# Kernel optimization log

Hardware: AMD Instinct MI355X
Metric: run time of the kernel (lower is better)

## Reference

```python
import jax, jax.numpy as jnp
import numpy as np

N_NODES = 100000
N_EDGES = 1600000
IN_F, HID_F, OUT_F = 64, 64, 16


def setup_inputs() -> dict:
    key = jax.random.key(0)
    k_x, k_e, k_w1, k_w2 = jax.random.split(key, 4)
    x = jax.random.normal(k_x, (N_NODES, IN_F), dtype=jnp.float32)
    edge_index = jax.random.randint(k_e, (2, N_EDGES), 0, N_NODES, dtype=jnp.int64)
    # Glorot-ish init for the GCNConv linear weights; bias zeros (PyG default)
    W1 = jax.random.normal(k_w1, (IN_F, HID_F), dtype=jnp.float32) / np.sqrt(IN_F)
    b1 = jnp.zeros((HID_F,), dtype=jnp.float32)
    W2 = jax.random.normal(k_w2, (HID_F, OUT_F), dtype=jnp.float32) / np.sqrt(HID_F)
    b2 = jnp.zeros((OUT_F,), dtype=jnp.float32)
    return {"x": x, "edge_index": edge_index, "W1": W1, "b1": b1, "W2": W2, "b2": b2}


def reference(x, edge_index, W1, b1, W2, b2):
    N = x.shape[0]
    # GCNConv: add self-loops, symmetric normalization D^-1/2 A D^-1/2
    loop = jnp.arange(N, dtype=edge_index.dtype)
    src = jnp.concatenate([edge_index[0], loop])  # [E+N]
    dst = jnp.concatenate([edge_index[1], loop])  # [E+N]
    deg = jax.ops.segment_sum(jnp.ones_like(dst, dtype=x.dtype), dst, num_segments=N)
    dis = jax.lax.rsqrt(deg)  # deg >= 1 due to self-loops
    norm = dis[src] * dis[dst]  # [E+N]

    def gcn_conv(h, W, b):
        h = h @ W                                   # [N, d_out]
        msg = h[src] * norm[:, None]                # gather + scale  [E+N, d_out]
        agg = jax.ops.segment_sum(msg, dst, num_segments=N)  # scatter-add
        return agg + b

    h = jax.nn.relu(gcn_conv(x, W1, b1))
    h = gcn_conv(h, W2, b2)
    return jax.nn.log_softmax(h, axis=1)
```

## Files before the change

kernel.cpp:

```cpp
#include <hip/hip_runtime.h>
#include <hip/hip_bf16.h>
#include <hip/hip_fp16.h>


#define F1 64
#define F2 16
#define NBKT 256
#define BSH 512
#define NPB 256
#define SBD 1024
#define STG 9216

typedef _Float16 f16x8 __attribute__((ext_vector_type(8)));
typedef _Float16 f16x4 __attribute__((ext_vector_type(4)));
typedef float f32x2 __attribute__((ext_vector_type(2)));
typedef float f32x4 __attribute__((ext_vector_type(4)));
typedef float f32x8 __attribute__((ext_vector_type(8)));

__device__ inline f32x8 shfl_xor_f32x8(f32x8 v, int off) {
  f32x8 r;
#pragma unroll
  for (int k = 0; k < 8; ++k) r[k] = __shfl_xor(v[k], off);
  return r;
}
__device__ inline f32x4 shfl_xor_f32x4(f32x4 v, int off) {
  f32x4 r;
#pragma unroll
  for (int k = 0; k < 4; ++k) r[k] = __shfl_xor(v[k], off);
  return r;
}

__device__ inline void acc_fp8x8(f32x2* a, uint2 v) {
  a[0] += __builtin_amdgcn_cvt_pk_f32_fp8((int)v.x, false);
  a[1] += __builtin_amdgcn_cvt_pk_f32_fp8((int)v.x, true);
  a[2] += __builtin_amdgcn_cvt_pk_f32_fp8((int)v.y, false);
  a[3] += __builtin_amdgcn_cvt_pk_f32_fp8((int)v.y, true);
}

__global__ void k_w(const float* __restrict__ W1, const float* __restrict__ W2,
                    const float* __restrict__ b1,
                    __half* __restrict__ W1T, __half* __restrict__ W2Tp,
                    float* __restrict__ b1p, int* __restrict__ bcur, int nb) {
  int t = threadIdx.x;
  for (int i = t; i < 64 * 64; i += 256) {
    int n = i >> 6, k = i & 63;
    W1T[i] = __float2half(W1[k * 64 + n]);
  }
  for (int i = t; i < 16 * 64; i += 256) {
    int j = i >> 6, p = i & 63;
    int fp = 16 * (p & 3) + (p >> 2);
    W2Tp[i] = __float2half(W2[fp * 16 + j]);
  }
  if (t < 64) b1p[t] = b1[16 * (t & 3) + (t >> 2)];
  if (t < nb) bcur[t] = t * STG;
}

__global__ void k_bscatter(const int* __restrict__ src, const int* __restrict__ dst,
                           int* __restrict__ bcur, int* __restrict__ tmp,
                           int E, int nb, int chunk) {
  __shared__ int h[NBKT];
  __shared__ int cur[NBKT];
  int t = threadIdx.x, sb = blockIdx.x;
  int beg = sb * chunk, end = min(beg + chunk, E);
  if (t < NBKT) h[t] = 0;
  __syncthreads();
  int e;
  for (e = beg + t * 4; e + 4 <= end; e += 4 * SBD) {
    int4 d4 = *(const int4*)(dst + e);
    atomicAdd(&h[d4.x >> 9], 1);
    atomicAdd(&h[d4.y >> 9], 1);
    atomicAdd(&h[d4.z >> 9], 1);
    atomicAdd(&h[d4.w >> 9], 1);
  }
  for (; e < end; ++e) atomicAdd(&h[dst[e] >> 9], 1);
  __syncthreads();
  if (t < nb) cur[t] = atomicAdd(&bcur[t], h[t]);
  __syncthreads();
  for (e = beg + t * 4; e + 4 <= end; e += 4 * SBD) {
    int4 d4 = *(const int4*)(dst + e);
    int4 s4 = *(const int4*)(src + e);
    int b, off;
    b = d4.x >> 9; off = atomicAdd(&cur[b], 1); tmp[off] = (s4.x << 9) | (d4.x & 511);
    b = d4.y >> 9; off = atomicAdd(&cur[b], 1); tmp[off] = (s4.y << 9) | (d4.y & 511);
    b = d4.z >> 9; off = atomicAdd(&cur[b], 1); tmp[off] = (s4.z << 9) | (d4.z & 511);
    b = d4.w >> 9; off = atomicAdd(&cur[b], 1); tmp[off] = (s4.w << 9) | (d4.w & 511);
  }
  for (; e < end; ++e) {
    int d = dst[e];
    int b = d >> 9;
    int off = atomicAdd(&cur[b], 1);
    tmp[off] = (src[e] << 9) | (d & 511);
  }
}

__global__ void k_cg2(const int* __restrict__ tmp, const int* __restrict__ bcur,
                      int* __restrict__ csr, int* __restrict__ rowptr,
                      float* __restrict__ dis,
                      const float* __restrict__ x, const __half* __restrict__ W1T,
                      unsigned char* __restrict__ h1, int N, int nb) {
  __shared__ int stage[STG];
  __shared__ int sc[BSH];
  __shared__ int cnt[BSH];
  __shared__ int lofs[BSH];
  __shared__ float dnode[BSH];
  int b = blockIdx.x, t = threadIdx.x;
  int lenb = bcur[b] - b * STG;
  if (t < NBKT) sc[t] = (t < nb) ? (bcur[t] - t * STG) : 0;
  __syncthreads();
  for (int off = 1; off < NBKT; off <<= 1) {
    int a = (t < NBKT && t >= off) ? sc[t - off] : 0;
    __syncthreads();
    if (t < NBKT) sc[t] += a;
    __syncthreads();
  }
  int beg = (b == 0) ? 0 : sc[b - 1];
  __syncthreads();
  int s0 = b * STG;
  int lim = lenb & ~3;
  for (int i = t * 4; i < lim; i += 4 * BSH)
    *(int4*)(stage + i) = *(const int4*)(tmp + s0 + i);
  {
    int r = lim + t;
    if (r < lenb) stage[r] = tmp[s0 + r];
  }
  cnt[t] = 0;
  __syncthreads();
  for (int i = t; i < lenb; i += BSH) atomicAdd(&cnt[stage[i] & (BSH - 1)], 1);
  __syncthreads();
  sc[t] = cnt[t];
  __syncthreads();
  for (int off = 1; off < BSH; off <<= 1) {
    int a = (t >= off) ? sc[t - off] : 0;
    __syncthreads();
    sc[t] += a;
    __syncthreads();
  }
  int excl = (t == 0) ? 0 : sc[t - 1];
  lofs[t] = excl;
  int n = b * BSH + t;
  float dn_t = rsqrtf((float)(cnt[t] + 1));
  dnode[t] = dn_t;
  if (n <= N) rowptr[n] = beg + excl;
  if (n < N) dis[n] = dn_t;
  cnt[t] = 0;
  __syncthreads();
  for (int i = t; i < lenb; i += BSH) {
    int p = stage[i];
    int l = p & (BSH - 1);
    int off = atomicAdd(&cnt[l], 1);
    csr[beg + lofs[l] + off] = p >> 9;
  }
  int wv = t >> 6, lane = t & 63;
  int m = lane & 15, q = lane >> 4;
  const _Float16* wt = (const _Float16*)W1T;
  f16x8 bf[4][2];
#pragma unroll
  for (int c = 0; c < 4; ++c)
#pragma unroll
    for (int kt = 0; kt < 2; ++kt)
      bf[c][kt] = *(const f16x8*)&wt[(c * 16 + m) * 64 + kt * 32 + q * 8];
#pragma unroll
  for (int it = 0; it < 4; ++it) {
    int lrow0 = wv * 64 + it * 16;
    int row0 = b * BSH + lrow0;
    int arow = min(row0 + m, N - 1);
    f16x8 a[2];
#pragma unroll
    for (int kt = 0; kt < 2; ++kt) {
      const float4* xp = (const float4*)(x + (size_t)arow * 64 + kt * 32 + q * 8);
      float4 u = xp[0], v = xp[1];
      a[kt][0] = (_Float16)u.x; a[kt][1] = (_Float16)u.y;
      a[kt][2] = (_Float16)u.z; a[kt][3] = (_Float16)u.w;
      a[kt][4] = (_Float16)v.x; a[kt][5] = (_Float16)v.y;
      a[kt][6] = (_Float16)v.z; a[kt][7] = (_Float16)v.w;
    }
    f32x4 acc[4] = {};
#pragma unroll
    for (int kt = 0; kt < 2; ++kt)
#pragma unroll
      for (int c = 0; c < 4; ++c)
        acc[c] = __builtin_amdgcn_mfma_f32_16x16x32_f16(a[kt], bf[c][kt], acc[c], 0, 0, 0);
#pragma unroll
    for (int r = 0; r < 4; ++r) {
      int lr = lrow0 + q * 4 + r;
      int nn = b * BSH + lr;
      if (nn < N) {
        float dn = dnode[lr];
        int d = __builtin_amdgcn_cvt_pk_fp8_f32(acc[0][r] * dn, acc[1][r] * dn, 0, false);
        d = __builtin_amdgcn_cvt_pk_fp8_f32(acc[2][r] * dn, acc[3][r] * dn, d, true);
        *(unsigned int*)(h1 + (size_t)nn * 64 + m * 4) = (unsigned)d;
      }
    }
  }
}

__global__ void k_agg1f(const unsigned char* __restrict__ h, const float* __restrict__ dis,
                        const int* __restrict__ rowptr, const int* __restrict__ csr,
                        const float* __restrict__ b1p, const __half* __restrict__ W2Tp,
                        __half* __restrict__ h2, int N) {
  int gt = blockIdx.x * blockDim.x + threadIdx.x;
  int w = gt >> 6;
  int lane = gt & 63;
  int half = lane >> 5;
  int sub = (lane >> 3) & 3;
  int fl = lane & 7;
  int n = w * 2 + half;
  if (n >= N) return;
  float dn = dis[n];
  float4 bu = *(const float4*)(b1p + fl * 8);
  float4 bv = *(const float4*)(b1p + fl * 8 + 4);
  const _Float16* wt = (const _Float16*)W2Tp;
  f16x8 wj[4];
#pragma unroll
  for (int i = 0; i < 4; ++i)
    wj[i] = *(const f16x8*)&wt[(sub * 4 + i) * 64 + fl * 8];
  f32x2 a0[4] = {}, a1[4] = {};
  if (sub == 0)
    acc_fp8x8(a0, *(const uint2*)&h[(size_t)n * 64 + fl * 8]);
  int beg = rowptr[n], end = rowptr[n + 1];
  int e = beg + sub;
  int sA = (e < end) ? csr[e] : -1;
  int sB = (e + 4 < end) ? csr[e + 4] : -1;
  while (sB >= 0) {
    int e2 = e + 8;
    int sC = (e2 < end) ? csr[e2] : -1;
    int sD = (e2 + 4 < end) ? csr[e2 + 4] : -1;
    uint2 v0 = *(const uint2*)&h[(size_t)sA * 64 + fl * 8];
    uint2 v1 = *(const uint2*)&h[(size_t)sB * 64 + fl * 8];
    acc_fp8x8(a0, v0);
    acc_fp8x8(a1, v1);
    sA = sC; sB = sD; e = e2;
  }
  if (sA >= 0)
    acc_fp8x8(a0, *(const uint2*)&h[(size_t)sA * 64 + fl * 8]);
  f32x8 acc;
#pragma unroll
  for (int k = 0; k < 4; ++k) {
    f32x2 s = a0[k] + a1[k];
    acc[2 * k] = s[0];
    acc[2 * k + 1] = s[1];
  }
  acc += shfl_xor_f32x8(acc, 8);
  acc += shfl_xor_f32x8(acc, 16);
  float bb[8] = {bu.x, bu.y, bu.z, bu.w, bv.x, bv.y, bv.z, bv.w};
  float hr[8];
#pragma unroll
  for (int k = 0; k < 8; ++k)
    hr[k] = fmaxf(fmaf(dn, acc[k], bb[k]), 0.f);
  float p[4];
#pragma unroll
  for (int i = 0; i < 4; ++i) {
    float s = 0.f;
#pragma unroll
    for (int k = 0; k < 8; ++k) s = fmaf(hr[k], (float)wj[i][k], s);
    s += __shfl_xor(s, 1);
    s += __shfl_xor(s, 2);
    s += __shfl_xor(s, 4);
    p[i] = s;
  }
  if (fl == 0) {
    f16x4 o;
#pragma unroll
    for (int i = 0; i < 4; ++i) o[i] = (_Float16)(p[i] * dn);
    *(f16x4*)((_Float16*)h2 + (size_t)n * 16 + sub * 4) = o;
  }
}

__global__ void k_agg2(const __half* __restrict__ h2, const float* __restrict__ dis,
                       const int* __restrict__ rowptr, const int* __restrict__ csr,
                       const float* __restrict__ b2, float* __restrict__ out, int N) {
  int gt = blockIdx.x * blockDim.x + threadIdx.x;
  int w = gt >> 6;
  int lane = gt & 63;
  int half = lane >> 5;
  int sub = (lane >> 2) & 7;
  int fl = lane & 3;
  int n = w * 2 + half;
  if (n >= N) return;
  const _Float16* hp = (const _Float16*)h2;
  f32x4 acc0 = {}, acc1 = {};
  if (sub == 0)
    acc0 = __builtin_convertvector(*(const f16x4*)&hp[(size_t)n * 16 + fl * 4], f32x4);
  int beg = rowptr[n], end = rowptr[n + 1];
  int e = beg + sub;
  int sA = (e < end) ? csr[e] : -1;
  int sB = (e + 8 < end) ? csr[e + 8] : -1;
  while (sB >= 0) {
    int e2 = e + 16;
    int sC = (e2 < end) ? csr[e2] : -1;
    int sD = (e2 + 8 < end) ? csr[e2 + 8] : -1;
    f16x4 v0 = *(const f16x4*)&hp[(size_t)sA * 16 + fl * 4];
    f16x4 v1 = *(const f16x4*)&hp[(size_t)sB * 16 + fl * 4];
    acc0 += __builtin_convertvector(v0, f32x4);
    acc1 += __builtin_convertvector(v1, f32x4);
    sA = sC; sB = sD; e = e2;
  }
  if (sA >= 0)
    acc0 += __builtin_convertvector(*(const f16x4*)&hp[(size_t)sA * 16 + fl * 4], f32x4);
  f32x4 acc = acc0 + acc1;
  acc += shfl_xor_f32x4(acc, 4);
  acc += shfl_xor_f32x4(acc, 8);
  acc += shfl_xor_f32x4(acc, 16);
  if (sub == 0) {
    float dn = dis[n];
    float4 bb = *(const float4*)(b2 + fl * 4);
    float v0 = fmaf(dn, acc[0], bb.x);
    float v1 = fmaf(dn, acc[1], bb.y);
    float v2 = fmaf(dn, acc[2], bb.z);
    float v3 = fmaf(dn, acc[3], bb.w);
    float m = fmaxf(fmaxf(v0, v1), fmaxf(v2, v3));
    m = fmaxf(m, __shfl_xor(m, 1));
    m = fmaxf(m, __shfl_xor(m, 2));
    float s2 = __expf(v0 - m) + __expf(v1 - m) + __expf(v2 - m) + __expf(v3 - m);
    s2 += __shfl_xor(s2, 1);
    s2 += __shfl_xor(s2, 2);
    float ls = m + __logf(s2);
    float4 o = {v0 - ls, v1 - ls, v2 - ls, v3 - ls};
    *(float4*)(out + (size_t)n * 16 + fl * 4) = o;
  }
}

extern "C" void kernel_launch(void* const* d_in, const int* in_sizes, int n_in,
                              void* d_out, int out_size, void* d_ws, size_t ws_size,
                              hipStream_t stream) {
  const float* x = (const float*)d_in[0];
  const int* ei = (const int*)d_in[1];
  const float* W1 = (const float*)d_in[2];
  const float* b1 = (const float*)d_in[3];
  const float* W2 = (const float*)d_in[4];
  const float* b2 = (const float*)d_in[5];
  float* out = (float*)d_out;

  int N = in_sizes[0] / F1;
  int E = in_sizes[1] / 2;
  const int* src = ei;
  const int* dst = ei + E;
  int nb = (N + BSH - 1) >> 9;
  int chunk = ((E + NPB - 1) / NPB + 3) & ~3;

  char* ws = (char*)d_ws;
  size_t o_w1t = 0;
  size_t o_w2t = o_w1t + 64 * 64 * 2;
  size_t o_b1p = (o_w2t + 16 * 64 * 2 + 255) & ~(size_t)255;
  size_t o_bcur = (o_b1p + 64 * 4 + 255) & ~(size_t)255;
  size_t o_dis = (o_bcur + NBKT * 4 + 255) & ~(size_t)255;
  size_t o_rowp = (o_dis + (size_t)N * 4 + 255) & ~(size_t)255;
  size_t o_tmp = (o_rowp + (size_t)(N + 1) * 4 + 255) & ~(size_t)255;
  size_t o_csr = (o_tmp + (size_t)nb * STG * 4 + 255) & ~(size_t)255;
  size_t o_h1 = (o_csr + (size_t)E * 4 + 255) & ~(size_t)255;
  size_t o_h2 = (o_h1 + (size_t)N * 64 + 255) & ~(size_t)255;

  __half* W1T = (__half*)(ws + o_w1t);
  __half* W2Tp = (__half*)(ws + o_w2t);
  float* b1p = (float*)(ws + o_b1p);
  int* bcur = (int*)(ws + o_bcur);
  float* dis = (float*)(ws + o_dis);
  int* rowptr = (int*)(ws + o_rowp);
  int* tmp = (int*)(ws + o_tmp);
  int* csr = (int*)(ws + o_csr);
  unsigned char* h1 = (unsigned char*)(ws + o_h1);
  __half* h2 = (__half*)(ws + o_h2);

  k_w<<<1, 256, 0, stream>>>(W1, W2, b1, W1T, W2Tp, b1p, bcur, nb);
  k_bscatter<<<NPB, SBD, 0, stream>>>(src, dst, bcur, tmp, E, nb, chunk);
  k_cg2<<<nb, BSH, 0, stream>>>(tmp, bcur, csr, rowptr, dis, x, W1T, h1, N, nb);
  int aw = (N + 1) / 2;
  k_agg1f<<<((size_t)aw * 64 + 255) / 256, 256, 0, stream>>>(h1, dis, rowptr, csr, b1p, W2Tp, h2, N);
  k_agg2<<<((size_t)aw * 64 + 255) / 256, 256, 0, stream>>>(h2, dis, rowptr, csr, b2, out, N);
}
```

Before: 182.9 us.

## Run X·W1 GEMM as extra blocks of the bucket-scatter kernel, rescale later

The layer-1 feature transform (x @ W1 via MFMA, stored as fp8) moves out of the CSR-build kernel. It now runs in extra blocks appended to the edge bucket-scatter launch, so the x reads overlap with the atomic-heavy scatter. Because degrees are not known yet, h1 is stored unscaled, and the CSR kernel later reads h1 back, multiplies each row by its dis value and re-quantizes to fp8 in place. This adds an extra read and write pass over h1 and a second fp8 rounding.

```diff
diff --git a/kernel.cpp b/kernel.cpp
--- a/kernel.cpp
+++ b/kernel.cpp
@@ -55,115 +55,26 @@
   if (t < nb) bcur[t] = t * STG;
 }
 
-__global__ void k_bscatter(const int* __restrict__ src, const int* __restrict__ dst,
-                           int* __restrict__ bcur, int* __restrict__ tmp,
-                           int E, int nb, int chunk) {
-  __shared__ int h[NBKT];
-  __shared__ int cur[NBKT];
+__global__ void k_sg(const int* __restrict__ src, const int* __restrict__ dst,
+                     int* __restrict__ bcur, int* __restrict__ tmp,
+                     int E, int nb, int chunk,
+                     const float* __restrict__ x, const __half* __restrict__ W1T,
+                     unsigned char* __restrict__ h1, int N) {
   int t = threadIdx.x, sb = blockIdx.x;
-  int beg = sb * chunk, end = min(beg + chunk, E);
-  if (t < NBKT) h[t] = 0;
-  __syncthreads();
-  int e;
-  for (e = beg + t * 4; e + 4 <= end; e += 4 * SBD) {
-    int4 d4 = *(const int4*)(dst + e);
-    atomicAdd(&h[d4.x >> 9], 1);
-    atomicAdd(&h[d4.y >> 9], 1);
-    atomicAdd(&h[d4.z >> 9], 1);
-    atomicAdd(&h[d4.w >> 9], 1);
-  }
-  for (; e < end; ++e) atomicAdd(&h[dst[e] >> 9], 1);
-  __syncthreads();
-  if (t < nb) cur[t] = atomicAdd(&bcur[t], h[t]);
-  __syncthreads();
-  for (e = beg + t * 4; e + 4 <= end; e += 4 * SBD) {
-    int4 d4 = *(const int4*)(dst + e);
-    int4 s4 = *(const int4*)(src + e);
-    int b, off;
-    b = d4.x >> 9; off = atomicAdd(&cur[b], 1); tmp[off] = (s4.x << 9) | (d4.x & 511);
-    b = d4.y >> 9; off = atomicAdd(&cur[b], 1); tmp[off] = (s4.y << 9) | (d4.y & 511);
-    b = d4.z >> 9; off = atomicAdd(&cur[b], 1); tmp[off] = (s4.z << 9) | (d4.z & 511);
-    b = d4.w >> 9; off = atomicAdd(&cur[b], 1); tmp[off] = (s4.w << 9) | (d4.w & 511);
-  }
-  for (; e < end; ++e) {
-    int d = dst[e];
-    int b = d >> 9;
-    int off = atomicAdd(&cur[b], 1);
-    tmp[off] = (src[e] << 9) | (d & 511);
-  }
-}
-
-__global__ void k_cg2(const int* __restrict__ tmp, const int* __restrict__ bcur,
-                      int* __restrict__ csr, int* __restrict__ rowptr,
-                      float* __restrict__ dis,
-                      const float* __restrict__ x, const __half* __restrict__ W1T,
-                      unsigned char* __restrict__ h1, int N, int nb) {
-  __shared__ int stage[STG];
-  __shared__ int sc[BSH];
-  __shared__ int cnt[BSH];
-  __shared__ int lofs[BSH];
-  __shared__ float dnode[BSH];
-  int b = blockIdx.x, t = threadIdx.x;
-  int lenb = bcur[b] - b * STG;
-  if (t < NBKT) sc[t] = (t < nb) ? (bcur[t] - t * STG) : 0;
-  __syncthreads();
-  for (int off = 1; off < NBKT; off <<= 1) {
-    int a = (t < NBKT && t >= off) ? sc[t - off] : 0;
-    __syncthreads();
-    if (t < NBKT) sc[t] += a;
-    __syncthreads();
-  }
-  int beg = (b == 0) ? 0 : sc[b - 1];
-  __syncthreads();
-  int s0 = b * STG;
-  int lim = lenb & ~3;
-  for (int i = t * 4; i < lim; i += 4 * BSH)
-    *(int4*)(stage + i) = *(const int4*)(tmp + s0 + i);
-  {
-    int r = lim + t;
-    if (r < lenb) stage[r] = tmp[s0 + r];
-  }
-  cnt[t] = 0;
-  __syncthreads();
-  for (int i = t; i < lenb; i += BSH) atomicAdd(&cnt[stage[i] & (BSH - 1)], 1);
-  __syncthreads();
-  sc[t] = cnt[t];
-  __syncthreads();
-  for (int off = 1; off < BSH; off <<= 1) {
-    int a = (t >= off) ? sc[t - off] : 0;
-    __syncthreads();
-    sc[t] += a;
-    __syncthreads();
-  }
-  int excl = (t == 0) ? 0 : sc[t - 1];
-  lofs[t] = excl;
-  int n = b * BSH + t;
-  float dn_t = rsqrtf((float)(cnt[t] + 1));
-  dnode[t] = dn_t;
-  if (n <= N) rowptr[n] = beg + excl;
-  if (n < N) dis[n] = dn_t;
-  cnt[t] = 0;
-  __syncthreads();
-  for (int i = t; i < lenb; i += BSH) {
-    int p = stage[i];
-    int l = p & (BSH - 1);
-    int off = atomicAdd(&cnt[l], 1);
-    csr[beg + lofs[l] + off] = p >> 9;
-  }
-  int wv = t >> 6, lane = t & 63;
-  int m = lane & 15, q = lane >> 4;
-  const _Float16* wt = (const _Float16*)W1T;
-  f16x8 bf[4][2];
-#pragma unroll
-  for (int c = 0; c < 4; ++c)
-#pragma unroll
-    for (int kt = 0; kt < 2; ++kt)
-      bf[c][kt] = *(const f16x8*)&wt[(c * 16 + m) * 64 + kt * 32 + q * 8];
-#pragma unroll
-  for (int it = 0; it < 4; ++it) {
-    int lrow0 = wv * 64 + it * 16;
-    int row0 = b * BSH + lrow0;
+  if (sb >= NPB) {
+    int g = sb - NPB;
+    int wv = t >> 6, lane = t & 63;
+    int m = lane & 15, q = lane >> 4;
+    int row0 = g * 256 + wv * 16;
+    if (row0 >= N) return;
     int arow = min(row0 + m, N - 1);
+    const _Float16* wt = (const _Float16*)W1T;
+    f16x8 bf[4][2];
+#pragma unroll
+    for (int c = 0; c < 4; ++c)
+#pragma unroll
+      for (int kt = 0; kt < 2; ++kt)
+        bf[c][kt] = *(const f16x8*)&wt[(c * 16 + m) * 64 + kt * 32 + q * 8];
     f16x8 a[2];
 #pragma unroll
     for (int kt = 0; kt < 2; ++kt) {
@@ -182,14 +93,117 @@
         acc[c] = __builtin_amdgcn_mfma_f32_16x16x32_f16(a[kt], bf[c][kt], acc[c], 0, 0, 0);
 #pragma unroll
     for (int r = 0; r < 4; ++r) {
-      int lr = lrow0 + q * 4 + r;
-      int nn = b * BSH + lr;
-      if (nn < N) {
-        float dn = dnode[lr];
-        int d = __builtin_amdgcn_cvt_pk_fp8_f32(acc[0][r] * dn, acc[1][r] * dn, 0, false);
-        d = __builtin_amdgcn_cvt_pk_fp8_f32(acc[2][r] * dn, acc[3][r] * dn, d, true);
-        *(unsigned int*)(h1 + (size_t)nn * 64 + m * 4) = (unsigned)d;
+      int n = row0 + q * 4 + r;
+      if (n < N) {
+        int d = __builtin_amdgcn_cvt_pk_fp8_f32(acc[0][r], acc[1][r], 0, false);
+        d = __builtin_amdgcn_cvt_pk_fp8_f32(acc[2][r], acc[3][r], d, true);
+        *(unsigned int*)(h1 + (size_t)n * 64 + m * 4) = (unsigned)d;
       }
+    }
+    return;
+  }
+  __shared__ int h[NBKT];
+  __shared__ int cur[NBKT];
+  int beg = sb * chunk, end = min(beg + chunk, E);
+  if (t < NBKT) h[t] = 0;
+  __syncthreads();
+  int e;
+  for (e = beg + t * 4; e + 4 <= end; e += 4 * SBD) {
+    int4 d4 = *(const int4*)(dst + e);
+    atomicAdd(&h[d4.x >> 9], 1);
+    atomicAdd(&h[d4.y >> 9], 1);
+    atomicAdd(&h[d4.z >> 9], 1);
+    atomicAdd(&h[d4.w >> 9], 1);
+  }
+  for (; e < end; ++e) atomicAdd(&h[dst[e] >> 9], 1);
+  __syncthreads();
+  if (t < nb) cur[t] = atomicAdd(&bcur[t], h[t]);
+  __syncthreads();
+  for (e = beg + t * 4; e + 4 <= end; e += 4 * SBD) {
+    int4 d4 = *(const int4*)(dst + e);
+    int4 s4 = *(const int4*)(src + e);
+    int b, off;
+    b = d4.x >> 9; off = atomicAdd(&cur[b], 1); tmp[off] = (s4.x << 9) | (d4.x & 511);
+    b = d4.y >> 9; off = atomicAdd(&cur[b], 1); tmp[off] = (s4.y << 9) | (d4.y & 511);
+    b = d4.z >> 9; off = atomicAdd(&cur[b], 1); tmp[off] = (s4.z << 9) | (d4.z & 511);
+    b = d4.w >> 9; off = atomicAdd(&cur[b], 1); tmp[off] = (s4.w << 9) | (d4.w & 511);
+  }
+  for (; e < end; ++e) {
+    int d = dst[e];
+    int b = d >> 9;
+    int off = atomicAdd(&cur[b], 1);
+    tmp[off] = (src[e] << 9) | (d & 511);
+  }
+}
+
+__global__ void k_csr(const int* __restrict__ tmp, const int* __restrict__ bcur,
+                      int* __restrict__ csr, int* __restrict__ rowptr,
+                      float* __restrict__ dis, unsigned char* __restrict__ h1,
+                      int N, int nb) {
+  __shared__ int stage[STG];
+  __shared__ int sc[BSH];
+  __shared__ int cnt[BSH];
+  __shared__ int lofs[BSH];
+  __shared__ float dnode[BSH];
+  int b = blockIdx.x, t = threadIdx.x;
+  int lenb = bcur[b] - b * STG;
+  if (t < NBKT) sc[t] = (t < nb) ? (bcur[t] - t * STG) : 0;
+  __syncthreads();
+  for (int off = 1; off < NBKT; off <<= 1) {
+    int a = (t < NBKT && t >= off) ? sc[t - off] : 0;
+    __syncthreads();
+    if (t < NBKT) sc[t] += a;
+    __syncthreads();
+  }
+  int beg = (b == 0) ? 0 : sc[b - 1];
+  __syncthreads();
+  int s0 = b * STG;
+  int lim = lenb & ~3;
+  for (int i = t * 4; i < lim; i += 4 * BSH)
+    *(int4*)(stage + i) = *(const int4*)(tmp + s0 + i);
+  {
+    int r = lim + t;
+    if (r < lenb) stage[r] = tmp[s0 + r];
+  }
+  cnt[t] = 0;
+  __syncthreads();
+  for (int i = t; i < lenb; i += BSH) atomicAdd(&cnt[stage[i] & (BSH - 1)], 1);
+  __syncthreads();
+  sc[t] = cnt[t];
+  __syncthreads();
+  for (int off = 1; off < BSH; off <<= 1) {
+    int a = (t >= off) ? sc[t - off] : 0;
+    __syncthreads();
+    sc[t] += a;
+    __syncthreads();
+  }
+  int excl = (t == 0) ? 0 : sc[t - 1];
+  lofs[t] = excl;
+  int n = b * BSH + t;
+  float dn_t = rsqrtf((float)(cnt[t] + 1));
+  dnode[t] = dn_t;
+  if (n <= N) rowptr[n] = beg + excl;
+  if (n < N) dis[n] = dn_t;
+  cnt[t] = 0;
+  __syncthreads();
+  for (int i = t; i < lenb; i += BSH) {
+    int p = stage[i];
+    int l = p & (BSH - 1);
+    int off = atomicAdd(&cnt[l], 1);
+    csr[beg + lofs[l] + off] = p >> 9;
+  }
+  for (int i = t; i < BSH * 16; i += BSH) {
+    int row = i >> 4, dw = i & 15;
+    int n2 = b * BSH + row;
+    if (n2 < N) {
+      float dnr = dnode[row];
+      unsigned int* hp = (unsigned int*)(h1 + ((size_t)n2 << 6));
+      unsigned v = hp[dw];
+      f32x2 lo = __builtin_amdgcn_cvt_pk_f32_fp8((int)v, false);
+      f32x2 hi = __builtin_amdgcn_cvt_pk_f32_fp8((int)v, true);
+      int d = __builtin_amdgcn_cvt_pk_fp8_f32(lo[0] * dnr, lo[1] * dnr, 0, false);
+      d = __builtin_amdgcn_cvt_pk_fp8_f32(hi[0] * dnr, hi[1] * dnr, d, true);
+      hp[dw] = (unsigned)d;
     }
   }
 }
@@ -361,9 +375,10 @@
   unsigned char* h1 = (unsigned char*)(ws + o_h1);
   __half* h2 = (__half*)(ws + o_h2);
 
+  int gb = (N + 255) / 256;
   k_w<<<1, 256, 0, stream>>>(W1, W2, b1, W1T, W2Tp, b1p, bcur, nb);
-  k_bscatter<<<NPB, SBD, 0, stream>>>(src, dst, bcur, tmp, E, nb, chunk);
-  k_cg2<<<nb, BSH, 0, stream>>>(tmp, bcur, csr, rowptr, dis, x, W1T, h1, N, nb);
+  k_sg<<<NPB + gb, SBD, 0, stream>>>(src, dst, bcur, tmp, E, nb, chunk, x, W1T, h1, N);
+  k_csr<<<nb, BSH, 0, stream>>>(tmp, bcur, csr, rowptr, dis, h1, N, nb);
   int aw = (N + 1) / 2;
   k_agg1f<<<((size_t)aw * 64 + 255) / 256, 256, 0, stream>>>(h1, dis, rowptr, csr, b1p, W2Tp, h2, N);
   k_agg2<<<((size_t)aw * 64 + 255) / 256, 256, 0, stream>>>(h2, dis, rowptr, csr, b2, out, N);
```

After: 191.2 us. 4.5% more time.
